# Kernel optimization log

Hardware: AMD Instinct MI355X
Metric: run time of the kernel (lower is better)

Reference implementation:

```python
import jax, jax.numpy as jnp
import numpy as np

N = 50000
E = 800000
D_IN = 128
H = 128
D_OUT = 64
BN_EPS = 1e-5


def setup_inputs() -> dict:
    key = jax.random.key(0)
    ks = jax.random.split(key, 20)

    def lin(k, fin, fout):
        kw, kb = jax.random.split(k)
        w = jax.random.normal(kw, (fin, fout), jnp.float32) / np.sqrt(fin)
        b = jnp.zeros((fout,), jnp.float32)
        return w, b

    def bn_params(k, d):
        kg, kb = jax.random.split(k)
        g = 1.0 + 0.1 * jax.random.normal(kg, (d,), jnp.float32)
        b = 0.1 * jax.random.normal(kb, (d,), jnp.float32)
        rm = 0.1 * jax.random.normal(jax.random.fold_in(k, 7), (d,), jnp.float32)
        rv = jnp.abs(1.0 + 0.1 * jax.random.normal(jax.random.fold_in(k, 9), (d,), jnp.float32))
        return g, b, rm, rv

    x = jax.random.normal(ks[0], (N, D_IN), jnp.float32)
    edge_index = jax.random.randint(ks[1], (2, E), 0, N, jnp.int64)
    ricci_curvature = jax.random.normal(ks[2], (E,), jnp.float32)

    W1, b1 = lin(ks[3], D_IN, H)
    Wc0, bc0 = lin(ks[4], H, H)          # convs[0]: hidden*1 -> hidden
    Wc1, bc1 = lin(ks[5], 2 * H, H)      # convs[1]: hidden*2 -> hidden
    Wout, bout = lin(ks[6], 3 * H, D_OUT)  # conv2: hidden*(L-1) -> out

    bn1_g, bn1_b, bn1_rm, bn1_rv = bn_params(ks[7], D_IN)
    bnc0_g, bnc0_b, bnc0_rm, bnc0_rv = bn_params(ks[8], H)
    bnc1_g, bnc1_b, bnc1_rm, bnc1_rv = bn_params(ks[9], 2 * H)
    bn2_g, bn2_b, bn2_rm, bn2_rv = bn_params(ks[10], 3 * H)

    return {
        "x": x, "edge_index": edge_index, "percent": 50,
        "ricci_curvature": ricci_curvature,
        "W1": W1, "b1": b1, "Wc0": Wc0, "bc0": bc0,
        "Wc1": Wc1, "bc1": bc1, "Wout": Wout, "bout": bout,
        "bn1_g": bn1_g, "bn1_b": bn1_b, "bn1_rm": bn1_rm, "bn1_rv": bn1_rv,
        "bnc0_g": bnc0_g, "bnc0_b": bnc0_b, "bnc0_rm": bnc0_rm, "bnc0_rv": bnc0_rv,
        "bnc1_g": bnc1_g, "bnc1_b": bnc1_b, "bnc1_rm": bnc1_rm, "bnc1_rv": bnc1_rv,
        "bn2_g": bn2_g, "bn2_b": bn2_b, "bn2_rm": bn2_rm, "bn2_rv": bn2_rv,
    }


def _bn_eval(h, g, b, rm, rv):
    # BatchNorm1d in eval mode: affine normalize with running stats.
    return (h - rm) * (g * jax.lax.rsqrt(rv + BN_EPS)) + b


def reference(x, edge_index, percent, ricci_curvature,
              W1, b1, Wc0, bc0, Wc1, bc1, Wout, bout,
              bn1_g, bn1_b, bn1_rm, bn1_rv,
              bnc0_g, bnc0_b, bnc0_rm, bnc0_rv,
              bnc1_g, bnc1_b, bnc1_rm, bnc1_rv,
              bn2_g, bn2_b, bn2_rm, bn2_rv):
    n = x.shape[0]
    # GCN normalization with self-loops (PyG GCNConv default), shared by all layers
    loops = jnp.arange(n, dtype=edge_index.dtype)
    row = jnp.concatenate([edge_index[0], loops])  # source
    col = jnp.concatenate([edge_index[1], loops])  # target
    deg = jax.ops.segment_sum(jnp.ones_like(col, dtype=x.dtype), col, num_segments=n)
    dinv = jax.lax.rsqrt(deg)  # deg >= 1 thanks to self loops
    norm = (dinv[row] * dinv[col])[:, None]  # [E+N, 1]

    def gcn(h, W, b):
        hw = h @ W                                   # transform first (PyG order)
        msg = hw[row] * norm                          # gather + scale per edge
        return jax.ops.segment_sum(msg, col, num_segments=n) + b

    # eval mode: no sampling / dynamic reweighting, dropout = identity
    h = _bn_eval(x, bn1_g, bn1_b, bn1_rm, bn1_rv)
    h = jax.nn.relu(gcn(h, W1, b1))
    r0 = h

    h = _bn_eval(h, bnc0_g, bnc0_b, bnc0_rm, bnc0_rv)
    h = jax.nn.relu(gcn(h, Wc0, bc0))
    r1 = h
    h = jnp.concatenate([r0, r1], axis=1)  # [N, 2H]

    h = _bn_eval(h, bnc1_g, bnc1_b, bnc1_rm, bnc1_rv)
    h = jax.nn.relu(gcn(h, Wc1, bc1))
    r2 = h
    h = jnp.concatenate([r0, r1, r2], axis=1)  # [N, 3H]

    h = _bn_eval(h, bn2_g, bn2_b, bn2_rm, bn2_rv)
    out = gcn(h, Wout, bout)
    return (out, r0, r1, r2)
```

## Files before the change

kernel.cpp:

```cpp
#include <hip/hip_runtime.h>
#include <hip/hip_bf16.h>
#include <stdint.h>

#define NN 50000
#define NE 800000

typedef unsigned short ushort8 __attribute__((ext_vector_type(8)));
typedef __bf16 bf16x8 __attribute__((ext_vector_type(8)));
typedef float f32x4 __attribute__((ext_vector_type(4)));

__device__ __forceinline__ float bf2f_bits(unsigned short u) {
  unsigned int x = ((unsigned int)u) << 16;
  float f;
  __builtin_memcpy(&f, &x, 4);
  return f;
}
__device__ __forceinline__ unsigned short f2bf_bits(float f) {
  unsigned int x;
  __builtin_memcpy(&x, &f, 4);
  unsigned int lsb = (x >> 16) & 1u;
  x += 0x7fffu + lsb;
  return (unsigned short)(x >> 16);
}
__device__ __forceinline__ float lo16(unsigned int v) { return bf2f_bits((unsigned short)v); }
__device__ __forceinline__ float hi16(unsigned int v) { return bf2f_bits((unsigned short)(v >> 16)); }
__device__ __forceinline__ float loadf(const void* base, size_t idx, int isbf) {
  if (isbf) return bf2f_bits(((const unsigned short*)base)[idx]);
  return ((const float*)base)[idx];
}

__global__ void k_sniff(const void* x, const void* ei, int* flags, int* cnt) {
  int i = blockIdx.x * 256 + threadIdx.x;
  if (i < NN) cnt[i] = 0;
  if (blockIdx.x != 0) return;
  __shared__ int badbf;
  __shared__ int zodd;
  int tid = threadIdx.x;
  if (tid == 0) { badbf = 0; zodd = 0; }
  __syncthreads();
  unsigned short u = ((const unsigned short*)x)[tid];
  float v = bf2f_bits(u);
  float av = fabsf(v);
  int ok = (av == 0.0f) || (av > 1e-8f && av < 1e8f);
  if (!ok) atomicAdd(&badbf, 1);
  int e32 = ((const int*)ei)[tid];
  if ((tid & 1) && e32 == 0) atomicAdd(&zodd, 1);
  __syncthreads();
  if (tid == 0) {
    flags[0] = (badbf <= 12) ? 1 : 0;
    flags[1] = (zodd >= 100) ? 1 : 0;
  }
}

__global__ void k_cvt_edges(const void* ei, int* erow, int* ecol, int* rank,
                            int* cnt, const int* flags) {
  int e = blockIdx.x * 256 + threadIdx.x;
  if (e >= NE) return;
  int r, c;
  if (flags[1]) {
    const long long* p = (const long long*)ei;
    r = (int)p[e];
    c = (int)p[NE + e];
  } else {
    const int* p = (const int*)ei;
    r = p[e];
    c = p[NE + e];
  }
  erow[e] = r;
  ecol[e] = c;
  rank[e] = atomicAdd(&cnt[c], 1);
}

__global__ void k_cvt_xb(const void* x, unsigned short* xb, const int* flags) {
  int i4 = (blockIdx.x * 256 + threadIdx.x) * 4;
  if (i4 >= NN * 128) return;
  int isbf = flags[0];
  if (isbf) {
    *reinterpret_cast<uint2*>(xb + i4) =
        *reinterpret_cast<const uint2*>((const unsigned short*)x + i4);
  } else {
    float4 v = *reinterpret_cast<const float4*>((const float*)x + i4);
    xb[i4 + 0] = f2bf_bits(v.x); xb[i4 + 1] = f2bf_bits(v.y);
    xb[i4 + 2] = f2bf_bits(v.z); xb[i4 + 3] = f2bf_bits(v.w);
  }
}

__global__ void k_scan1(const int* cnt, int* indptr, int* bsum, float* dinv, int n) {
  __shared__ int sm[256];
  int tid = threadIdx.x;
  int i = blockIdx.x * 256 + tid;
  int v = (i < n) ? cnt[i] : 0;
  if (i < n) dinv[i] = rsqrtf((float)(v + 1));
  sm[tid] = v;
  __syncthreads();
  for (int off = 1; off < 256; off <<= 1) {
    int t = (tid >= off) ? sm[tid - off] : 0;
    __syncthreads();
    sm[tid] += t;
    __syncthreads();
  }
  if (i < n) indptr[i] = sm[tid] - v;
  if (tid == 255) bsum[blockIdx.x] = sm[255];
}
__global__ void k_scan2(int* bsum, int nb) {
  __shared__ int sm[256];
  int tid = threadIdx.x;
  int v = (tid < nb) ? bsum[tid] : 0;
  sm[tid] = v;
  __syncthreads();
  for (int off = 1; off < 256; off <<= 1) {
    int t = (tid >= off) ? sm[tid - off] : 0;
    __syncthreads();
    sm[tid] += t;
    __syncthreads();
  }
  if (tid < nb) bsum[tid] = sm[tid] - v;
  if (tid == 0) bsum[nb] = sm[255];
}
__global__ void k_scan3(int* indptr, const int* bsum, int n, int nb) {
  int i = blockIdx.x * 256 + threadIdx.x;
  if (i < n) indptr[i] += bsum[i >> 8];
  else if (i == n) indptr[n] = bsum[nb];
}
__global__ void k_fill(const int* erow, const int* ecol, const int* rank,
                       const int* indptr, int* srcs) {
  int e = blockIdx.x * 256 + threadIdx.x;
  if (e >= NE) return;
  srcs[indptr[ecol[e]] + rank[e]] = erow[e];
}

__global__ void k_prep_wt_all(
    const void* W1, const void* Wc0, const void* Wc1, const void* Wout,
    const void* g1, const void* g2, const void* g3, const void* g4,
    const void* rv1, const void* rv2, const void* rv3, const void* rv4,
    unsigned short* Wtb, const int* flags) {
  int idx = blockIdx.x * 256 + threadIdx.x;
  if (idx >= 90112) return;
  int isbf = flags[0];
  const void *W, *g, *rv;
  int K, NOUT, base;
  if (idx < 16384)      { W = W1;   g = g1; rv = rv1; K = 128; NOUT = 128; base = 0; }
  else if (idx < 32768) { W = Wc0;  g = g2; rv = rv2; K = 128; NOUT = 128; base = 16384; }
  else if (idx < 65536) { W = Wc1;  g = g3; rv = rv3; K = 256; NOUT = 128; base = 32768; }
  else                  { W = Wout; g = g4; rv = rv4; K = 384; NOUT = 64;  base = 65536; }
  int li = idx - base;
  int j = li / K, k = li % K;
  float s = loadf(g, k, isbf) * rsqrtf(loadf(rv, k, isbf) + 1e-5f);
  Wtb[idx] = f2bf_bits(s * loadf(W, (size_t)k * NOUT + j, isbf));
}
__global__ void k_prep_c_all(
    const void* W1, const void* Wc0, const void* Wc1, const void* Wout,
    const void* g1, const void* g2, const void* g3, const void* g4,
    const void* b1, const void* b2, const void* b3, const void* b4,
    const void* rm1, const void* rm2, const void* rm3, const void* rm4,
    const void* rv1, const void* rv2, const void* rv3, const void* rv4,
    float* cvec, const int* flags) {
  int jj = blockIdx.x;
  int lane = threadIdx.x;
  int isbf = flags[0];
  const void *W, *g, *bb, *rm, *rv;
  int K, NOUT, j;
  if (jj < 128)      { W = W1;   g = g1; bb = b1; rm = rm1; rv = rv1; K = 128; NOUT = 128; j = jj; }
  else if (jj < 256) { W = Wc0;  g = g2; bb = b2; rm = rm2; rv = rv2; K = 128; NOUT = 128; j = jj - 128; }
  else if (jj < 384) { W = Wc1;  g = g3; bb = b3; rm = rm3; rv = rv3; K = 256; NOUT = 128; j = jj - 256; }
  else               { W = Wout; g = g4; bb = b4; rm = rm4; rv = rv4; K = 384; NOUT = 64;  j = jj - 384; }
  float acc = 0.f;
  for (int k = lane; k < K; k += 64) {
    float s = loadf(g, k, isbf) * rsqrtf(loadf(rv, k, isbf) + 1e-5f);
    float t = loadf(bb, k, isbf) - loadf(rm, k, isbf) * s;
    acc += t * loadf(W, (size_t)k * NOUT + j, isbf);
  }
#pragma unroll
  for (int off = 32; off; off >>= 1) acc += __shfl_down(acc, off);
  if (lane == 0) cvec[jj] = acc;
}

template <int NOUT, int K>
__global__ __launch_bounds__(256) void k_gemm_mfma(
    const unsigned short* __restrict__ h0b, const unsigned short* __restrict__ h1b,
    const unsigned short* __restrict__ h2b,
    const unsigned short* __restrict__ h0d, const unsigned short* __restrict__ h1d,
    const unsigned short* __restrict__ h2d,
    const unsigned short* __restrict__ Wtb,
    const float* __restrict__ cvec, const float* __restrict__ dinv,
    unsigned short* __restrict__ hb, const int* __restrict__ flags) {
  constexpr int KS = K / 32;
  constexpr int NT = NOUT / 16;
  int isbf = flags[0];
  const unsigned short* h0 = (isbf && h0d) ? h0d : h0b;
  const unsigned short* h1 = (isbf && h1d) ? h1d : h1b;
  const unsigned short* h2 = (isbf && h2d) ? h2d : h2b;
  int tid = threadIdx.x;
  int wv = tid >> 6, lane = tid & 63;
  int row0 = blockIdx.x * 64 + wv * 16;
  int l15 = lane & 15;
  int kq = lane >> 4;
  int arow = row0 + l15;
  bool inb = arow < NN;

  bf16x8 afrag[KS];
#pragma unroll
  for (int ks = 0; ks < KS; ++ks) {
    int kg = ks * 32 + kq * 8;
    const unsigned short* src = (kg >> 7) == 0 ? h0 : ((kg >> 7) == 1 ? h1 : h2);
    ushort8 u = (ushort8)0;
    if (inb) u = *reinterpret_cast<const ushort8*>(src + (size_t)arow * 128 + (kg & 127));
    afrag[ks] = __builtin_bit_cast(bf16x8, u);
  }

  f32x4 acc[NT];
#pragma unroll
  for (int nt = 0; nt < NT; ++nt) acc[nt] = (f32x4)0.f;

#pragma unroll
  for (int nt = 0; nt < NT; ++nt) {
    const unsigned short* wrow = Wtb + (size_t)(nt * 16 + l15) * K + kq * 8;
#pragma unroll
    for (int ks = 0; ks < KS; ++ks) {
      ushort8 u = *reinterpret_cast<const ushort8*>(wrow + ks * 32);
      acc[nt] = __builtin_amdgcn_mfma_f32_16x16x32_bf16(
          afrag[ks], __builtin_bit_cast(bf16x8, u), acc[nt], 0, 0, 0);
    }
  }

  int orow0 = row0 + kq * 4;
  float dv[4];
  bool ob[4];
#pragma unroll
  for (int r = 0; r < 4; ++r) {
    int orow = orow0 + r;
    ob[r] = orow < NN;
    dv[r] = ob[r] ? dinv[orow] : 0.f;
  }
#pragma unroll
  for (int nt = 0; nt < NT; ++nt) {
    int col = nt * 16 + l15;
    float cv = cvec[col];
#pragma unroll
    for (int r = 0; r < 4; ++r) {
      if (ob[r])
        hb[(size_t)(orow0 + r) * NOUT + col] = f2bf_bits(dv[r] * (acc[nt][r] + cv));
    }
  }
}

template <bool RELU>
__global__ __launch_bounds__(256) void k_agg128(
    const unsigned short* __restrict__ hb, const int* __restrict__ indptr,
    const int* __restrict__ srcs, const float* __restrict__ dinv,
    const void* __restrict__ bias, void* __restrict__ dout, size_t region_off,
    unsigned short* __restrict__ rb, const int* __restrict__ flags) {
  int gw = __builtin_amdgcn_readfirstlane(blockIdx.x * 4 + (threadIdx.x >> 6));
  int lane = threadIdx.x & 63;
  if (gw >= NN) return;
  int isbf = flags[0];
  int e0 = indptr[gw], e1 = indptr[gw + 1];
  size_t co = (size_t)lane * 2;
  unsigned int sv = *reinterpret_cast<const unsigned int*>(hb + (size_t)gw * 128 + co);
  float a0 = lo16(sv), a1 = hi16(sv);
  float b0 = 0.f, b1 = 0.f, c0 = 0.f, c1 = 0.f, d0 = 0.f, d1 = 0.f;
  int e = e0;
  for (; e + 7 < e1; e += 8) {
    int s0 = srcs[e], s1 = srcs[e + 1], s2 = srcs[e + 2], s3 = srcs[e + 3];
    int s4 = srcs[e + 4], s5 = srcs[e + 5], s6 = srcs[e + 6], s7 = srcs[e + 7];
    unsigned int v0 = *reinterpret_cast<const unsigned int*>(hb + (size_t)s0 * 128 + co);
    unsigned int v1 = *reinterpret_cast<const unsigned int*>(hb + (size_t)s1 * 128 + co);
    unsigned int v2 = *reinterpret_cast<const unsigned int*>(hb + (size_t)s2 * 128 + co);
    unsigned int v3 = *reinterpret_cast<const unsigned int*>(hb + (size_t)s3 * 128 + co);
    unsigned int v4 = *reinterpret_cast<const unsigned int*>(hb + (size_t)s4 * 128 + co);
    unsigned int v5 = *reinterpret_cast<const unsigned int*>(hb + (size_t)s5 * 128 + co);
    unsigned int v6 = *reinterpret_cast<const unsigned int*>(hb + (size_t)s6 * 128 + co);
    unsigned int v7 = *reinterpret_cast<const unsigned int*>(hb + (size_t)s7 * 128 + co);
    a0 += lo16(v0); a1 += hi16(v0); b0 += lo16(v1); b1 += hi16(v1);
    c0 += lo16(v2); c1 += hi16(v2); d0 += lo16(v3); d1 += hi16(v3);
    a0 += lo16(v4); a1 += hi16(v4); b0 += lo16(v5); b1 += hi16(v5);
    c0 += lo16(v6); c1 += hi16(v6); d0 += lo16(v7); d1 += hi16(v7);
  }
  for (; e < e1; ++e) {
    int s0 = srcs[e];
    unsigned int v0 = *reinterpret_cast<const unsigned int*>(hb + (size_t)s0 * 128 + co);
    a0 += lo16(v0); a1 += hi16(v0);
  }
  float dv = dinv[gw];
  float o0 = dv * ((a0 + b0) + (c0 + d0)) + loadf(bias, co + 0, isbf);
  float o1 = dv * ((a1 + b1) + (c1 + d1)) + loadf(bias, co + 1, isbf);
  if (RELU) { o0 = fmaxf(o0, 0.f); o1 = fmaxf(o1, 0.f); }
  size_t eo = region_off + (size_t)gw * 128 + co;
  if (isbf) {
    unsigned int pk = (unsigned int)f2bf_bits(o0) | ((unsigned int)f2bf_bits(o1) << 16);
    *reinterpret_cast<unsigned int*>((unsigned short*)dout + eo) = pk;
  } else {
    float2 fo; fo.x = o0; fo.y = o1;
    *reinterpret_cast<float2*>((float*)dout + eo) = fo;
    unsigned int pk = (unsigned int)f2bf_bits(o0) | ((unsigned int)f2bf_bits(o1) << 16);
    *reinterpret_cast<unsigned int*>(rb + (size_t)gw * 128 + co) = pk;
  }
}

__global__ __launch_bounds__(256) void k_agg64out(
    const unsigned short* __restrict__ hb, const int* __restrict__ indptr,
    const int* __restrict__ srcs, const float* __restrict__ dinv,
    const void* __restrict__ bias, void* __restrict__ dout,
    const int* __restrict__ flags) {
  int gw = blockIdx.x * 8 + (threadIdx.x >> 5);
  int lane = threadIdx.x & 31;
  if (gw >= NN) return;
  int isbf = flags[0];
  int e0 = indptr[gw], e1 = indptr[gw + 1];
  int e = e0;
  size_t co = (size_t)lane * 2;
  unsigned int sv = *reinterpret_cast<const unsigned int*>(hb + (size_t)gw * 64 + co);
  float a0 = lo16(sv), a1 = hi16(sv);
  float b0 = 0.f, b1 = 0.f, c0 = 0.f, c1 = 0.f, d0 = 0.f, d1 = 0.f;
  for (; e + 3 < e1; e += 4) {
    int sa = srcs[e], sb = srcs[e + 1], sc = srcs[e + 2], sd = srcs[e + 3];
    unsigned int va = *reinterpret_cast<const unsigned int*>(hb + (size_t)sa * 64 + co);
    unsigned int vb = *reinterpret_cast<const unsigned int*>(hb + (size_t)sb * 64 + co);
    unsigned int vc = *reinterpret_cast<const unsigned int*>(hb + (size_t)sc * 64 + co);
    unsigned int vd = *reinterpret_cast<const unsigned int*>(hb + (size_t)sd * 64 + co);
    a0 += lo16(va); a1 += hi16(va); b0 += lo16(vb); b1 += hi16(vb);
    c0 += lo16(vc); c1 += hi16(vc); d0 += lo16(vd); d1 += hi16(vd);
  }
  for (; e < e1; ++e) {
    int sa = srcs[e];
    unsigned int va = *reinterpret_cast<const unsigned int*>(hb + (size_t)sa * 64 + co);
    a0 += lo16(va); a1 += hi16(va);
  }
  float dv = dinv[gw];
  float o0 = dv * ((a0 + b0) + (c0 + d0)) + loadf(bias, co + 0, isbf);
  float o1 = dv * ((a1 + b1) + (c1 + d1)) + loadf(bias, co + 1, isbf);
  size_t eo = (size_t)gw * 64 + co;
  if (isbf) {
    unsigned int pk = (unsigned int)f2bf_bits(o0) | ((unsigned int)f2bf_bits(o1) << 16);
    *reinterpret_cast<unsigned int*>((unsigned short*)dout + eo) = pk;
  } else {
    float2 fo; fo.x = o0; fo.y = o1;
    *reinterpret_cast<float2*>((float*)dout + eo) = fo;
  }
}

extern "C" void kernel_launch(void* const* d_in, const int* in_sizes, int n_in,
                              void* d_out, int out_size, void* d_ws, size_t ws_size,
                              hipStream_t stream) {
  const void* x    = d_in[0];
  const void* ei   = d_in[1];
  const void* W1   = d_in[4];
  const void* b1   = d_in[5];
  const void* Wc0  = d_in[6];
  const void* bc0  = d_in[7];
  const void* Wc1  = d_in[8];
  const void* bc1  = d_in[9];
  const void* Wout = d_in[10];
  const void* bout = d_in[11];
  const void *bn1g = d_in[12], *bn1b = d_in[13], *bn1rm = d_in[14], *bn1rv = d_in[15];
  const void *bc0g = d_in[16], *bc0b = d_in[17], *bc0rm = d_in[18], *bc0rv = d_in[19];
  const void *bc1g = d_in[20], *bc1b = d_in[21], *bc1rm = d_in[22], *bc1rv = d_in[23];
  const void *bn2g = d_in[24], *bn2b = d_in[25], *bn2rm = d_in[26], *bn2rv = d_in[27];
  (void)in_sizes; (void)n_in; (void)out_size; (void)ws_size;

  char* w = (char*)d_ws;
  auto carve = [&](size_t bytes) {
    char* p = w;
    w += (bytes + 255) & ~(size_t)255;
    return p;
  };
  int*   flags  = (int*)  carve(256);
  float* dinv   = (float*)carve(sizeof(float) * NN);
  int*   cnt    = (int*)  carve(sizeof(int) * NN);
  int*   indptr = (int*)  carve(sizeof(int) * (NN + 1));
  int*   bsum   = (int*)  carve(sizeof(int) * 256);
  int*   erow   = (int*)  carve(sizeof(int) * NE);
  int*   ecol   = (int*)  carve(sizeof(int) * NE);
  int*   rank   = (int*)  carve(sizeof(int) * NE);
  int*   srcs   = (int*)  carve(sizeof(int) * NE);
  unsigned short* Wtb = (unsigned short*)carve(sizeof(short) * 90112);
  float* cvec   = (float*)carve(sizeof(float) * 448);
  unsigned short* xb  = (unsigned short*)carve(sizeof(short) * (size_t)NN * 128);
  unsigned short* hb  = (unsigned short*)carve(sizeof(short) * (size_t)NN * 128);
  unsigned short* rb0 = (unsigned short*)carve(sizeof(short) * (size_t)NN * 128);
  unsigned short* rb1 = (unsigned short*)carve(sizeof(short) * (size_t)NN * 128);
  unsigned short* rb2 = (unsigned short*)carve(sizeof(short) * (size_t)NN * 128);

  const int gN = (NN + 255) / 256;
  const int gE = (NE + 255) / 256;
  const int nb = (NN + 255) / 256;
  const int gG = (NN + 63) / 64;
  const int gA2 = (NN + 3) / 4;
  const int gA1 = (NN + 7) / 8;

  k_sniff<<<gN, 256, 0, stream>>>(x, ei, flags, cnt);
  k_cvt_edges<<<gE, 256, 0, stream>>>(ei, erow, ecol, rank, cnt, flags);
  k_cvt_xb<<<(NN * 128 / 4 + 255) / 256, 256, 0, stream>>>(x, xb, flags);
  k_scan1<<<nb, 256, 0, stream>>>(cnt, indptr, bsum, dinv, NN);
  k_scan2<<<1, 256, 0, stream>>>(bsum, nb);
  k_scan3<<<(NN + 1 + 255) / 256, 256, 0, stream>>>(indptr, bsum, NN, nb);
  k_fill<<<gE, 256, 0, stream>>>(erow, ecol, rank, indptr, srcs);
  k_prep_wt_all<<<(90112 + 255) / 256, 256, 0, stream>>>(
      W1, Wc0, Wc1, Wout, bn1g, bc0g, bc1g, bn2g, bn1rv, bc0rv, bc1rv, bn2rv, Wtb, flags);
  k_prep_c_all<<<448, 64, 0, stream>>>(
      W1, Wc0, Wc1, Wout, bn1g, bc0g, bc1g, bn2g, bn1b, bc0b, bc1b, bn2b,
      bn1rm, bc0rm, bc1rm, bn2rm, bn1rv, bc0rv, bc1rv, bn2rv, cvec, flags);

  const size_t offO  = 0;
  const size_t offR0 = (size_t)NN * 64;
  const size_t offR1 = offR0 + (size_t)NN * 128;
  const size_t offR2 = offR1 + (size_t)NN * 128;
  unsigned short* d0 = (unsigned short*)d_out;

  k_gemm_mfma<128, 128><<<gG, 256, 0, stream>>>(
      xb, nullptr, nullptr, nullptr, nullptr, nullptr, Wtb + 0, cvec + 0, dinv, hb, flags);
  k_agg128<true><<<gA2, 256, 0, stream>>>(hb, indptr, srcs, dinv, b1, d_out, offR0, rb0, flags);

  k_gemm_mfma<128, 128><<<gG, 256, 0, stream>>>(
      rb0, nullptr, nullptr, d0 + offR0, nullptr, nullptr, Wtb + 16384, cvec + 128, dinv, hb, flags);
  k_agg128<true><<<gA2, 256, 0, stream>>>(hb, indptr, srcs, dinv, bc0, d_out, offR1, rb1, flags);

  k_gemm_mfma<128, 256><<<gG, 256, 0, stream>>>(
      rb0, rb1, nullptr, d0 + offR0, d0 + offR1, nullptr, Wtb + 32768, cvec + 256, dinv, hb, flags);
  k_agg128<true><<<gA2, 256, 0, stream>>>(hb, indptr, srcs, dinv, bc1, d_out, offR2, rb2, flags);

  k_gemm_mfma<64, 384><<<gG, 256, 0, stream>>>(
      rb0, rb1, rb2, d0 + offR0, d0 + offR1, d0 + offR2, Wtb + 65536, cvec + 384, dinv, hb, flags);
  k_agg64out<<<gA1, 256, 0, stream>>>(hb, indptr, srcs, dinv, bout, d_out, flags);
}
```

Measured before the change: 334.4 us.

## Partition CSR fill scatter by XCD and skip bf16 input copy

The CSR fill scatter is split in two. A first pass computes each edge's destination position. A second pass launches 8 groups of blocks, selected by blockIdx&7, and each group writes only destinations in its own 100k-entry range. The intent is to keep scattered writes local to one XCD's L2, at the cost of every group rereading all positions (8x reads). Separately, the x conversion kernel now exits early for bf16 input and the first GEMM is handed the raw x pointer, which saves a copy, assuming the GEMM uses that pointer when the bf16 flag is set.

```diff
diff --git a/kernel.cpp b/kernel.cpp
--- a/kernel.cpp
+++ b/kernel.cpp
@@ -4,6 +4,9 @@
 
 #define NN 50000
 #define NE 800000
+#define PR 100000
+#define ESL 4096
+#define NSL ((NE + ESL - 1) / ESL)
 
 typedef unsigned short ushort8 __attribute__((ext_vector_type(8)));
 typedef __bf16 bf16x8 __attribute__((ext_vector_type(8)));
@@ -72,17 +75,12 @@
 }
 
 __global__ void k_cvt_xb(const void* x, unsigned short* xb, const int* flags) {
+  if (flags[0]) return;
   int i4 = (blockIdx.x * 256 + threadIdx.x) * 4;
   if (i4 >= NN * 128) return;
-  int isbf = flags[0];
-  if (isbf) {
-    *reinterpret_cast<uint2*>(xb + i4) =
-        *reinterpret_cast<const uint2*>((const unsigned short*)x + i4);
-  } else {
-    float4 v = *reinterpret_cast<const float4*>((const float*)x + i4);
-    xb[i4 + 0] = f2bf_bits(v.x); xb[i4 + 1] = f2bf_bits(v.y);
-    xb[i4 + 2] = f2bf_bits(v.z); xb[i4 + 3] = f2bf_bits(v.w);
-  }
+  float4 v = *reinterpret_cast<const float4*>((const float*)x + i4);
+  xb[i4 + 0] = f2bf_bits(v.x); xb[i4 + 1] = f2bf_bits(v.y);
+  xb[i4 + 2] = f2bf_bits(v.z); xb[i4 + 3] = f2bf_bits(v.w);
 }
 
 __global__ void k_scan1(const int* cnt, int* indptr, int* bsum, float* dinv, int n) {
@@ -122,11 +120,23 @@
   if (i < n) indptr[i] += bsum[i >> 8];
   else if (i == n) indptr[n] = bsum[nb];
 }
-__global__ void k_fill(const int* erow, const int* ecol, const int* rank,
-                       const int* indptr, int* srcs) {
+__global__ void k_pos(const int* ecol, const int* rank, const int* indptr, int* pos) {
   int e = blockIdx.x * 256 + threadIdx.x;
-  if (e >= NE) return;
-  srcs[indptr[ecol[e]] + rank[e]] = erow[e];
+  if (e < NE) pos[e] = indptr[ecol[e]] + rank[e];
+}
+__global__ __launch_bounds__(256) void k_fill_xcd(
+    const int* __restrict__ erow, const int* __restrict__ pos,
+    int* __restrict__ srcs) {
+  int xcd = blockIdx.x & 7;
+  int slice = blockIdx.x >> 3;
+  int p0 = xcd * PR;
+  int p1 = min(p0 + PR, NE);
+  int base = slice * ESL;
+  int end = min(base + ESL, NE);
+  for (int e = base + threadIdx.x; e < end; e += 256) {
+    int p = pos[e];
+    if (p >= p0 && p < p1) srcs[p] = erow[e];
+  }
 }
 
 __global__ void k_prep_wt_all(
@@ -372,6 +382,7 @@
   int*   erow   = (int*)  carve(sizeof(int) * NE);
   int*   ecol   = (int*)  carve(sizeof(int) * NE);
   int*   rank   = (int*)  carve(sizeof(int) * NE);
+  int*   pos    = (int*)  carve(sizeof(int) * NE);
   int*   srcs   = (int*)  carve(sizeof(int) * NE);
   unsigned short* Wtb = (unsigned short*)carve(sizeof(short) * 90112);
   float* cvec   = (float*)carve(sizeof(float) * 448);
@@ -394,7 +405,8 @@
   k_scan1<<<nb, 256, 0, stream>>>(cnt, indptr, bsum, dinv, NN);
   k_scan2<<<1, 256, 0, stream>>>(bsum, nb);
   k_scan3<<<(NN + 1 + 255) / 256, 256, 0, stream>>>(indptr, bsum, NN, nb);
-  k_fill<<<gE, 256, 0, stream>>>(erow, ecol, rank, indptr, srcs);
+  k_pos<<<gE, 256, 0, stream>>>(ecol, rank, indptr, pos);
+  k_fill_xcd<<<NSL * 8, 256, 0, stream>>>(erow, pos, srcs);
   k_prep_wt_all<<<(90112 + 255) / 256, 256, 0, stream>>>(
       W1, Wc0, Wc1, Wout, bn1g, bc0g, bc1g, bn2g, bn1rv, bc0rv, bc1rv, bn2rv, Wtb, flags);
   k_prep_c_all<<<448, 64, 0, stream>>>(
@@ -408,7 +420,8 @@
   unsigned short* d0 = (unsigned short*)d_out;
 
   k_gemm_mfma<128, 128><<<gG, 256, 0, stream>>>(
-      xb, nullptr, nullptr, nullptr, nullptr, nullptr, Wtb + 0, cvec + 0, dinv, hb, flags);
+      xb, nullptr, nullptr, (const unsigned short*)x, nullptr, nullptr,
+      Wtb + 0, cvec + 0, dinv, hb, flags);
   k_agg128<true><<<gA2, 256, 0, stream>>>(hb, indptr, srcs, dinv, b1, d_out, offR0, rb0, flags);
 
   k_gemm_mfma<128, 128><<<gG, 256, 0, stream>>>(
```

Result: no change. 341.1 us (+2.0%).

## Shard degree-count atomics per XCC and skip bf16 input copy

Applied to the files above, without the earlier changes.

Degree counting now uses eight per-XCC counter arrays selected by the hardware XCC id, which avoids cross-die atomic contention on one counter per node. The rank carries the shard id in its high bits, and the scan turns the per-shard counts into offsets that the CSR fill adds back. Separately, when the input is already bf16 the conversion copy is skipped and the first GEMM reads x directly. This costs an 8x larger counter buffer to zero and extra reads in the scan and fill.

```diff
diff --git a/kernel.cpp b/kernel.cpp
--- a/kernel.cpp
+++ b/kernel.cpp
@@ -29,9 +29,9 @@
   return ((const float*)base)[idx];
 }
 
-__global__ void k_sniff(const void* x, const void* ei, int* flags, int* cnt) {
+__global__ void k_sniff(const void* x, const void* ei, int* flags, int* cnt8) {
   int i = blockIdx.x * 256 + threadIdx.x;
-  if (i < NN) cnt[i] = 0;
+  if (i < 8 * NN) cnt8[i] = 0;
   if (blockIdx.x != 0) return;
   __shared__ int badbf;
   __shared__ int zodd;
@@ -53,9 +53,12 @@
 }
 
 __global__ void k_cvt_edges(const void* ei, int* erow, int* ecol, int* rank,
-                            int* cnt, const int* flags) {
+                            int* cnt8, const int* flags) {
   int e = blockIdx.x * 256 + threadIdx.x;
   if (e >= NE) return;
+  unsigned int xcc;
+  asm volatile("s_getreg_b32 %0, hwreg(HW_REG_XCC_ID)" : "=s"(xcc));
+  xcc &= 7;
   int r, c;
   if (flags[1]) {
     const long long* p = (const long long*)ei;
@@ -68,29 +71,35 @@
   }
   erow[e] = r;
   ecol[e] = c;
-  rank[e] = atomicAdd(&cnt[c], 1);
+  int rl = atomicAdd(&cnt8[xcc * NN + c], 1);
+  rank[e] = rl | (int)(xcc << 27);
 }
 
 __global__ void k_cvt_xb(const void* x, unsigned short* xb, const int* flags) {
+  if (flags[0]) return;
   int i4 = (blockIdx.x * 256 + threadIdx.x) * 4;
   if (i4 >= NN * 128) return;
-  int isbf = flags[0];
-  if (isbf) {
-    *reinterpret_cast<uint2*>(xb + i4) =
-        *reinterpret_cast<const uint2*>((const unsigned short*)x + i4);
-  } else {
-    float4 v = *reinterpret_cast<const float4*>((const float*)x + i4);
-    xb[i4 + 0] = f2bf_bits(v.x); xb[i4 + 1] = f2bf_bits(v.y);
-    xb[i4 + 2] = f2bf_bits(v.z); xb[i4 + 3] = f2bf_bits(v.w);
-  }
-}
-
-__global__ void k_scan1(const int* cnt, int* indptr, int* bsum, float* dinv, int n) {
+  float4 v = *reinterpret_cast<const float4*>((const float*)x + i4);
+  xb[i4 + 0] = f2bf_bits(v.x); xb[i4 + 1] = f2bf_bits(v.y);
+  xb[i4 + 2] = f2bf_bits(v.z); xb[i4 + 3] = f2bf_bits(v.w);
+}
+
+__global__ void k_scan1(int* cnt8, int* indptr, int* bsum, float* dinv, int n) {
   __shared__ int sm[256];
   int tid = threadIdx.x;
   int i = blockIdx.x * 256 + tid;
-  int v = (i < n) ? cnt[i] : 0;
-  if (i < n) dinv[i] = rsqrtf((float)(v + 1));
+  int v = 0;
+  if (i < n) {
+    int run = 0;
+#pragma unroll
+    for (int s = 0; s < 8; ++s) {
+      int cs = cnt8[s * NN + i];
+      cnt8[s * NN + i] = run;
+      run += cs;
+    }
+    v = run;
+    dinv[i] = rsqrtf((float)(v + 1));
+  }
   sm[tid] = v;
   __syncthreads();
   for (int off = 1; off < 256; off <<= 1) {
@@ -123,10 +132,13 @@
   else if (i == n) indptr[n] = bsum[nb];
 }
 __global__ void k_fill(const int* erow, const int* ecol, const int* rank,
-                       const int* indptr, int* srcs) {
+                       const int* indptr, const int* cnt8, int* srcs) {
   int e = blockIdx.x * 256 + threadIdx.x;
   if (e >= NE) return;
-  srcs[indptr[ecol[e]] + rank[e]] = erow[e];
+  int c = ecol[e];
+  int rk = rank[e];
+  int sh = (unsigned int)rk >> 27;
+  srcs[indptr[c] + cnt8[sh * NN + c] + (rk & 0x07FFFFFF)] = erow[e];
 }
 
 __global__ void k_prep_wt_all(
@@ -366,7 +378,7 @@
   };
   int*   flags  = (int*)  carve(256);
   float* dinv   = (float*)carve(sizeof(float) * NN);
-  int*   cnt    = (int*)  carve(sizeof(int) * NN);
+  int*   cnt8   = (int*)  carve(sizeof(int) * 8 * NN);
   int*   indptr = (int*)  carve(sizeof(int) * (NN + 1));
   int*   bsum   = (int*)  carve(sizeof(int) * 256);
   int*   erow   = (int*)  carve(sizeof(int) * NE);
@@ -381,20 +393,20 @@
   unsigned short* rb1 = (unsigned short*)carve(sizeof(short) * (size_t)NN * 128);
   unsigned short* rb2 = (unsigned short*)carve(sizeof(short) * (size_t)NN * 128);
 
-  const int gN = (NN + 255) / 256;
+  const int gN8 = (8 * NN + 255) / 256;
   const int gE = (NE + 255) / 256;
   const int nb = (NN + 255) / 256;
   const int gG = (NN + 63) / 64;
   const int gA2 = (NN + 3) / 4;
   const int gA1 = (NN + 7) / 8;
 
-  k_sniff<<<gN, 256, 0, stream>>>(x, ei, flags, cnt);
-  k_cvt_edges<<<gE, 256, 0, stream>>>(ei, erow, ecol, rank, cnt, flags);
+  k_sniff<<<gN8, 256, 0, stream>>>(x, ei, flags, cnt8);
+  k_cvt_edges<<<gE, 256, 0, stream>>>(ei, erow, ecol, rank, cnt8, flags);
   k_cvt_xb<<<(NN * 128 / 4 + 255) / 256, 256, 0, stream>>>(x, xb, flags);
-  k_scan1<<<nb, 256, 0, stream>>>(cnt, indptr, bsum, dinv, NN);
+  k_scan1<<<nb, 256, 0, stream>>>(cnt8, indptr, bsum, dinv, NN);
   k_scan2<<<1, 256, 0, stream>>>(bsum, nb);
   k_scan3<<<(NN + 1 + 255) / 256, 256, 0, stream>>>(indptr, bsum, NN, nb);
-  k_fill<<<gE, 256, 0, stream>>>(erow, ecol, rank, indptr, srcs);
+  k_fill<<<gE, 256, 0, stream>>>(erow, ecol, rank, indptr, cnt8, srcs);
   k_prep_wt_all<<<(90112 + 255) / 256, 256, 0, stream>>>(
       W1, Wc0, Wc1, Wout, bn1g, bc0g, bc1g, bn2g, bn1rv, bc0rv, bc1rv, bn2rv, Wtb, flags);
   k_prep_c_all<<<448, 64, 0, stream>>>(
@@ -408,7 +420,8 @@
   unsigned short* d0 = (unsigned short*)d_out;
 
   k_gemm_mfma<128, 128><<<gG, 256, 0, stream>>>(
-      xb, nullptr, nullptr, nullptr, nullptr, nullptr, Wtb + 0, cvec + 0, dinv, hb, flags);
+      xb, nullptr, nullptr, (const unsigned short*)x, nullptr, nullptr,
+      Wtb + 0, cvec + 0, dinv, hb, flags);
   k_agg128<true><<<gA2, 256, 0, stream>>>(hb, indptr, srcs, dinv, b1, d_out, offR0, rb0, flags);
 
   k_gemm_mfma<128, 128><<<gG, 256, 0, stream>>>(
```

Measured after the change: 333.5 us. Within noise of the previous version (-0.3%).
